# Kernel optimization log

Measured on AMD Instinct MI355X. Metric: run time of the kernel, lower is better.

Reference implementation:

```python
import jax, jax.numpy as jnp
import numpy as np

B, S, D = 4, 2048, 1024
H = 16
HD = D // H  # 64

def setup_inputs() -> dict:
    key = jax.random.key(0)
    ks = jax.random.split(key, 4)
    scale = 0.02
    return {
        "hidden_states": jax.random.normal(ks[0], (B, S, D), dtype=jnp.float32),
        "attention_mask": jnp.zeros((B, 1, 1, S), dtype=jnp.float32),
        "Wq": jax.random.normal(ks[1], (D, D), dtype=jnp.float32) * scale,
        "bq": jnp.zeros((D,), dtype=jnp.float32),
        "Wk": jax.random.normal(ks[2], (D, D), dtype=jnp.float32) * scale,
        "bk": jnp.zeros((D,), dtype=jnp.float32),
        "Wv": jax.random.normal(ks[3], (D, D), dtype=jnp.float32) * scale,
        "bv": jnp.zeros((D,), dtype=jnp.float32),
    }

def reference(hidden_states, attention_mask, Wq, bq, Wk, bk, Wv, bv):
    b, s, d = hidden_states.shape
    def proj(W, bias):
        # Linear then split heads: [b, s, d] -> [b, H, s, HD]
        y = hidden_states @ W.T + bias
        return y.reshape(b, s, H, HD).transpose(0, 2, 1, 3)
    Q = proj(Wq, bq)
    K = proj(Wk, bk)
    V = proj(Wv, bv)
    scores = jnp.einsum('bhqd,bhkd->bhqk', Q, K) / jnp.sqrt(jnp.float32(HD))
    scores = scores + attention_mask  # additive mask, broadcast [b,1,1,s]
    probs = jax.nn.softmax(scores, axis=-1)
    # dropout prob = 0.0 (eval-mode): identity
    context = jnp.einsum('bhqk,bhkd->bhqd', probs, V)
    return context.transpose(0, 2, 1, 3).reshape(b, s, d)
```

## Files before the change

kernel.cpp:

```cpp
#include <hip/hip_runtime.h>


typedef short bf16x4 __attribute__((ext_vector_type(4)));
typedef short bf16x8 __attribute__((ext_vector_type(8)));
typedef float f32x4 __attribute__((ext_vector_type(4)));

#define SEQ 2048
#define DIM 1024
#define NH 16
#define HDIM 64
#define QKV_ELEMS ((size_t)64 * SEQ * HDIM)

#define WS_FLAG  50331648ull
#define WS_XBF   50331904ull
#define WS_WBF   67109120ull
#define WS_BF32  73400576ull
#define WS_NEED  73412868ull

#define LOG2E 1.4426950408889634f
#define QSCALE (0.125f * LOG2E)

static __device__ __forceinline__ unsigned short f2bf(float f) {
  union { float f; unsigned u; } x; x.f = f;
  unsigned r = x.u + 0x7fffu + ((x.u >> 16) & 1u);
  return (unsigned short)(r >> 16);
}
static __device__ __forceinline__ float bf2f(unsigned short h) {
  union { unsigned u; float f; } x; x.u = ((unsigned)h) << 16;
  return x.f;
}
static __device__ __forceinline__ unsigned cvtpk(float a, float b) {
  unsigned r;
  asm("v_cvt_pk_bf16_f32 %0, %1, %2" : "=v"(r) : "v"(a), "v"(b));
  return r;
}
static __device__ __forceinline__ int vswz(int s) {
  return (s & ~31) | (((s >> 2) & 3) << 3) | (((s >> 4) & 1) << 2);
}

template <bool FP32>
static __device__ __forceinline__ float load1(const void* p, size_t i) {
  if (FP32) return ((const float*)p)[i];
  else      return bf2f(((const unsigned short*)p)[i]);
}
template <bool FP32>
static __device__ __forceinline__ bf16x8 load8bf(const void* p, size_t i) {
  if (FP32) {
    f32x4 a = *(const f32x4*)((const float*)p + i);
    f32x4 b = *(const f32x4*)((const float*)p + i + 4);
    union { bf16x8 v; unsigned short u[8]; } r;
#pragma unroll
    for (int j = 0; j < 4; ++j) { r.u[j] = f2bf(a[j]); r.u[4 + j] = f2bf(b[j]); }
    return r.v;
  } else {
    return *(const bf16x8*)((const unsigned short*)p + i);
  }
}
static __device__ __forceinline__ bf16x8 load8bf_rt(const void* p, size_t i, bool fp32) {
  return fp32 ? load8bf<true>(p, i) : load8bf<false>(p, i);
}

static __device__ __forceinline__ void glds16(const unsigned short* g, unsigned short* l) {
  __builtin_amdgcn_global_load_lds(
      (const __attribute__((address_space(1))) unsigned int*)(unsigned long long)(const void*)g,
      (__attribute__((address_space(3))) unsigned int*)(unsigned int)(unsigned long long)(void*)l,
      16, 0, 0);
}

__global__ void detect_dtype(const unsigned short* __restrict__ X, int* __restrict__ flag) {
  __shared__ int zc[1024], bc[1024];
  int z = 0, b = 0;
  for (int i = threadIdx.x; i < 4096; i += 1024) {
    unsigned short u = X[8 * i];
    if (u == 0) z++;
    int e = (u >> 7) & 0xff;
    if (e >= 134) b++;
  }
  zc[threadIdx.x] = z; bc[threadIdx.x] = b;
  __syncthreads();
  for (int s = 512; s > 0; s >>= 1) {
    if (threadIdx.x < s) { zc[threadIdx.x] += zc[threadIdx.x + s]; bc[threadIdx.x] += bc[threadIdx.x + s]; }
    __syncthreads();
  }
  if (threadIdx.x == 0)
    *flag = (zc[0] > 2048 || bc[0] > 16) ? 1 : 0;
}

__global__ void convert_all_u(const void* __restrict__ X,
                              const void* __restrict__ Wq, const void* __restrict__ Wk,
                              const void* __restrict__ Wv,
                              const void* __restrict__ bq, const void* __restrict__ bk,
                              const void* __restrict__ bv,
                              unsigned char* __restrict__ ws, const int* __restrict__ flag) {
  const bool fp32 = (*flag != 0);
  unsigned short* Xb = (unsigned short*)(ws + WS_XBF);
  unsigned short* Wb = (unsigned short*)(ws + WS_WBF);
  float* Bb = (float*)(ws + WS_BF32);
  int blk = blockIdx.x;
  if (blk < 4096) {
    size_t base = ((size_t)blk * 256 + threadIdx.x) * 8;
    *(bf16x8*)(Xb + base) = load8bf_rt(X, base, fp32);
  } else if (blk < 5632) {
    int w = (blk - 4096) >> 9;
    int r = (blk - 4096) & 511;
    const void* W = (w == 0) ? Wq : (w == 1) ? Wk : Wv;
    size_t base = ((size_t)r * 256 + threadIdx.x) * 8;
    *(bf16x8*)(Wb + (size_t)w * 1048576 + base) = load8bf_rt(W, base, fp32);
  } else {
    int w = blk - 5632;
    const void* Bsrc = (w == 0) ? bq : (w == 1) ? bk : bv;
    for (int i = threadIdx.x; i < 1024; i += 256)
      Bb[w * 1024 + i] = fp32 ? load1<true>(Bsrc, i) : load1<false>(Bsrc, i);
  }
}

__global__ __launch_bounds__(256) void qkv_bf(
    const unsigned short* __restrict__ Xb, const unsigned short* __restrict__ Wb,
    const float* __restrict__ Bb,
    unsigned short* __restrict__ Qo, unsigned short* __restrict__ Ko,
    unsigned short* __restrict__ Vo)
{
  const int bid = blockIdx.x;
  const int wg  = (bid & 7) * 192 + (bid >> 3);
  const int z   = wg / 512;
  const int rem = wg - z * 512;
  const int nb  = rem >> 6;
  const int mb  = rem & 63;
  const unsigned short* W = Wb + (size_t)z * 1048576;

  __shared__ __align__(16) unsigned short Xs[128 * 64];
  __shared__ __align__(16) unsigned short Ws[128 * 64];

  const int tid  = threadIdx.x;
  const int wave = tid >> 6;
  const int lane = tid & 63;
  const int col  = lane & 15;
  const int quad = lane >> 4;
  const int wr = wave & 1;
  const int wc = wave >> 1;
  const int m0 = mb * 128;
  const int n0 = nb * 128;

  f32x4 zero4 = {0.f, 0.f, 0.f, 0.f};
  f32x4 acc[4][4];
#pragma unroll
  for (int i = 0; i < 4; ++i)
#pragma unroll
    for (int j = 0; j < 4; ++j) acc[i][j] = zero4;

  const int srow8 = lane >> 3;
  const int sseg  = lane & 7;

  for (int k0 = 0; k0 < DIM; k0 += 64) {
    __syncthreads();
#pragma unroll
    for (int a = 0; a < 4; ++a) {
      int rowbase = wave * 32 + a * 8;
      int row = rowbase + srow8;
      int lseg = sseg ^ (row & 7);
      glds16(Xb + (size_t)(m0 + row) * DIM + k0 + lseg * 8, Xs + rowbase * 64);
      glds16(W  + (size_t)(n0 + row) * DIM + k0 + lseg * 8, Ws + rowbase * 64);
    }
    __syncthreads();

#pragma unroll
    for (int kk = 0; kk < 2; ++kk) {
      bf16x8 Af[4], Bf[4];
#pragma unroll
      for (int i = 0; i < 4; ++i) {
        int ra = wr * 64 + i * 16 + col;
        Af[i] = *(const bf16x8*)(Xs + ra * 64 + ((kk * 4 + quad) ^ (ra & 7)) * 8);
        int rb = wc * 64 + i * 16 + col;
        Bf[i] = *(const bf16x8*)(Ws + rb * 64 + ((kk * 4 + quad) ^ (rb & 7)) * 8);
      }
#pragma unroll
      for (int i = 0; i < 4; ++i)
#pragma unroll
        for (int j = 0; j < 4; ++j)
          acc[i][j] = __builtin_amdgcn_mfma_f32_16x16x32_bf16(Af[i], Bf[j], acc[i][j], 0, 0, 0);
    }
  }

  const float oscale = (z == 0) ? QSCALE : 1.0f;
  if (z < 2) {
    unsigned short* Yo = (z == 0) ? Qo : Ko;
#pragma unroll
    for (int i = 0; i < 4; ++i) {
#pragma unroll
      for (int j = 0; j < 4; ++j) {
        int n = n0 + wc * 64 + j * 16 + col;
        float bvf = Bb[z * 1024 + n];
        int h = n >> 6, hd = n & 63;
#pragma unroll
        for (int r = 0; r < 4; ++r) {
          int m = m0 + wr * 64 + i * 16 + quad * 4 + r;
          int b = m >> 11, s = m & 2047;
          Yo[((size_t)(b * NH + h) * SEQ + s) * HDIM + hd] = f2bf((acc[i][j][r] + bvf) * oscale);
        }
      }
    }
  } else {
#pragma unroll
    for (int i = 0; i < 4; ++i) {
#pragma unroll
      for (int j = 0; j < 4; ++j) {
        int n = n0 + wc * 64 + j * 16 + col;
        float bvf = Bb[2 * 1024 + n];
        int h = n >> 6, hd = n & 63;
        int mbase = m0 + wr * 64 + i * 16 + quad * 4;
        int b = mbase >> 11, s = mbase & 2047;
        unsigned long long pk = 0;
#pragma unroll
        for (int r = 0; r < 4; ++r)
          pk |= (unsigned long long)f2bf(acc[i][j][r] + bvf) << (16 * r);
        *(unsigned long long*)(Vo + ((size_t)(b * NH + h) * HDIM + hd) * SEQ + vswz(s)) = pk;
      }
    }
  }
}

#define XS_STRIDE 40
template <bool FP32>
__global__ __launch_bounds__(256) void qkv_any(
    const void* __restrict__ X,
    const void* __restrict__ Wq, const void* __restrict__ bq,
    const void* __restrict__ Wk, const void* __restrict__ bk,
    const void* __restrict__ Wv, const void* __restrict__ bv,
    unsigned short* __restrict__ Qo, unsigned short* __restrict__ Ko,
    unsigned short* __restrict__ Vo, const int* __restrict__ flag)
{
  if (*flag != (FP32 ? 1 : 0)) return;
  const int z = blockIdx.z;
  const void* W    = (z == 0) ? Wq : (z == 1) ? Wk : Wv;
  const void* bias = (z == 0) ? bq : (z == 1) ? bk : bv;

  __shared__ __align__(16) unsigned short Xs[128 * XS_STRIDE];
  __shared__ __align__(16) unsigned short Ws[128 * XS_STRIDE];

  const int tid  = threadIdx.x;
  const int wave = tid >> 6;
  const int lane = tid & 63;
  const int col  = lane & 15;
  const int quad = lane >> 4;
  const int wr = wave & 1;
  const int wc = wave >> 1;
  const int m0 = blockIdx.x * 128;
  const int n0 = blockIdx.y * 128;

  f32x4 zero4 = {0.f, 0.f, 0.f, 0.f};
  f32x4 acc[4][4];
#pragma unroll
  for (int i = 0; i < 4; ++i)
#pragma unroll
    for (int j = 0; j < 4; ++j) acc[i][j] = zero4;

  const int srow = tid >> 2;
  const int sseg = (tid & 3) << 3;

  for (int k0 = 0; k0 < DIM; k0 += 32) {
    __syncthreads();
#pragma unroll
    for (int a = 0; a < 2; ++a) {
      int r = a * 64 + srow;
      *(bf16x8*)(Xs + r * XS_STRIDE + sseg) = load8bf<FP32>(X, (size_t)(m0 + r) * DIM + k0 + sseg);
      *(bf16x8*)(Ws + r * XS_STRIDE + sseg) = load8bf<FP32>(W, (size_t)(n0 + r) * DIM + k0 + sseg);
    }
    __syncthreads();

    bf16x8 Af[4], Bf[4];
#pragma unroll
    for (int i = 0; i < 4; ++i)
      Af[i] = *(const bf16x8*)(Xs + (wr * 64 + i * 16 + col) * XS_STRIDE + quad * 8);
#pragma unroll
    for (int j = 0; j < 4; ++j)
      Bf[j] = *(const bf16x8*)(Ws + (wc * 64 + j * 16 + col) * XS_STRIDE + quad * 8);
#pragma unroll
    for (int i = 0; i < 4; ++i)
#pragma unroll
      for (int j = 0; j < 4; ++j)
        acc[i][j] = __builtin_amdgcn_mfma_f32_16x16x32_bf16(Af[i], Bf[j], acc[i][j], 0, 0, 0);
  }

  const float oscale = (z == 0) ? QSCALE : 1.0f;
  if (z < 2) {
    unsigned short* Yo = (z == 0) ? Qo : Ko;
#pragma unroll
    for (int i = 0; i < 4; ++i) {
#pragma unroll
      for (int j = 0; j < 4; ++j) {
        int n = n0 + wc * 64 + j * 16 + col;
        float bvf = load1<FP32>(bias, n);
        int h = n >> 6, hd = n & 63;
#pragma unroll
        for (int r = 0; r < 4; ++r) {
          int m = m0 + wr * 64 + i * 16 + quad * 4 + r;
          int b = m >> 11, s = m & 2047;
          Yo[((size_t)(b * NH + h) * SEQ + s) * HDIM + hd] = f2bf((acc[i][j][r] + bvf) * oscale);
        }
      }
    }
  } else {
#pragma unroll
    for (int i = 0; i < 4; ++i) {
#pragma unroll
      for (int j = 0; j < 4; ++j) {
        int n = n0 + wc * 64 + j * 16 + col;
        float bvf = load1<FP32>(bias, n);
        int h = n >> 6, hd = n & 63;
        int mbase = m0 + wr * 64 + i * 16 + quad * 4;
        int b = mbase >> 11, s = mbase & 2047;
        unsigned long long pk = 0;
#pragma unroll
        for (int r = 0; r < 4; ++r)
          pk |= (unsigned long long)f2bf(acc[i][j][r] + bvf) << (16 * r);
        *(unsigned long long*)(Vo + ((size_t)(b * NH + h) * HDIM + hd) * SEQ + vswz(s)) = pk;
      }
    }
  }
}

__global__ __launch_bounds__(512, 2) void attn_kernel(
    const unsigned short* __restrict__ Q,
    const unsigned short* __restrict__ K,
    const unsigned short* __restrict__ Vt,
    const void* __restrict__ mask,
    void* __restrict__ OutV, const int* __restrict__ flag)
{
  const bool fp32 = (*flag != 0);

  __shared__ __align__(16) unsigned short Ks[2 * 128 * 64];
  __shared__ __align__(16) unsigned short Vs[2 * 64 * 128];
  __shared__ __align__(16) float Msall[SEQ];

  const int tid  = threadIdx.x;
  const int wave = tid >> 6;
  const int lane = tid & 63;
  const int col  = lane & 15;
  const int quad = lane >> 4;
  const int qt = blockIdx.x;
  const int bh = blockIdx.y;
  const int b  = bh >> 4;
  const int h  = bh & 15;

  const unsigned short* Qb = Q  + (size_t)bh * SEQ * HDIM;
  const unsigned short* Kb = K  + (size_t)bh * SEQ * HDIM;
  const unsigned short* Vb = Vt + (size_t)bh * HDIM * SEQ;

  {
    if (fp32) {
      f32x4 a = *(const f32x4*)((const float*)mask + (size_t)b * SEQ + tid * 4);
#pragma unroll
      for (int j = 0; j < 4; ++j) a[j] *= LOG2E;
      *(f32x4*)(Msall + tid * 4) = a;
    } else {
      bf16x4 v = *(const bf16x4*)((const unsigned short*)mask + (size_t)b * SEQ + tid * 4);
      f32x4 a;
#pragma unroll
      for (int j = 0; j < 4; ++j) a[j] = bf2f((unsigned short)v[j]) * LOG2E;
      *(f32x4*)(Msall + tid * 4) = a;
    }
  }

  const int qrow0 = qt * 256 + wave * 32 + col;
  const int qrow1 = qrow0 + 16;
  const bf16x8 Qf00 = *(const bf16x8*)(Qb + (size_t)qrow0 * HDIM + quad * 8);
  const bf16x8 Qf01 = *(const bf16x8*)(Qb + (size_t)qrow0 * HDIM + 32 + quad * 8);
  const bf16x8 Qf10 = *(const bf16x8*)(Qb + (size_t)qrow1 * HDIM + quad * 8);
  const bf16x8 Qf11 = *(const bf16x8*)(Qb + (size_t)qrow1 * HDIM + 32 + quad * 8);

  const f32x4 z4 = {0.f, 0.f, 0.f, 0.f};
  f32x4 Oacc0[4], Oacc1[4];
  f32x4 Osum0 = z4, Osum1 = z4;
#pragma unroll
  for (int t = 0; t < 4; ++t) { Oacc0[t] = z4; Oacc1[t] = z4; }
  float mrun0 = -1e30f, mrun1 = -1e30f;

  union { bf16x8 v; unsigned u[4]; } ones;
#pragma unroll
  for (int i = 0; i < 4; ++i) ones.u[i] = 0x3F803F80u;

  const int krow_in = lane >> 3;
  const int kphys   = lane & 7;
  const int klseg   = kphys ^ krow_in;
  const unsigned short* kSrc0 = Kb + (size_t)(wave * 16 + 0 + krow_in) * HDIM + klseg * 8;
  const unsigned short* kSrc1 = Kb + (size_t)(wave * 16 + 8 + krow_in) * HDIM + klseg * 8;
  const int vrow_in = lane >> 4;
  const int vphys   = lane & 15;
  const int vrowA0  = wave * 8 + 0 + vrow_in;
  const int vrowA1  = wave * 8 + 4 + vrow_in;
  const unsigned short* vSrc0 = Vb + (size_t)vrowA0 * SEQ + (vphys ^ (vrowA0 & 15)) * 8;
  const unsigned short* vSrc1 = Vb + (size_t)vrowA1 * SEQ + (vphys ^ (vrowA1 & 15)) * 8;

  auto stage = [&](int ktn, int bufn) {
    unsigned short* Kdst = Ks + bufn * (128 * 64) + (wave * 16) * 64;
    unsigned short* Vdst = Vs + bufn * (64 * 128) + (wave * 8) * 128;
    const size_t ko = (size_t)ktn * 128 * HDIM;
    const size_t vo = (size_t)ktn * 128;
    glds16(kSrc0 + ko, Kdst);
    glds16(kSrc1 + ko, Kdst + 8 * 64);
    glds16(vSrc0 + vo, Vdst);
    glds16(vSrc1 + vo, Vdst + 4 * 128);
  };

  stage(0, 0);

  for (int kt = 0; kt < 16; ++kt) {
    __syncthreads();
    if (kt < 15) stage(kt + 1, (kt + 1) & 1);

    const unsigned short* Kcur = Ks + (kt & 1) * (128 * 64);
    const unsigned short* Vcur = Vs + (kt & 1) * (64 * 128);
    const float* Mc = Msall + kt * 128;

    f32x4 st0[8], st1[8];
    __builtin_amdgcn_s_setprio(1);
#pragma unroll
    for (int t = 0; t < 8; ++t) {
      const unsigned short* kr = Kcur + (t * 16 + col) * 64;
      bf16x8 Ka = *(const bf16x8*)(kr + (quad ^ (col & 7)) * 8);
      bf16x8 Kc = *(const bf16x8*)(kr + ((4 + quad) ^ (col & 7)) * 8);
      f32x4 c = *(const f32x4*)(Mc + t * 16 + quad * 4);
      f32x4 d0 = c, d1 = c;
      d0 = __builtin_amdgcn_mfma_f32_16x16x32_bf16(Ka, Qf00, d0, 0, 0, 0);
      d0 = __builtin_amdgcn_mfma_f32_16x16x32_bf16(Kc, Qf01, d0, 0, 0, 0);
      d1 = __builtin_amdgcn_mfma_f32_16x16x32_bf16(Ka, Qf10, d1, 0, 0, 0);
      d1 = __builtin_amdgcn_mfma_f32_16x16x32_bf16(Kc, Qf11, d1, 0, 0, 0);
      st0[t] = d0; st1[t] = d1;
    }
    __builtin_amdgcn_s_setprio(0);

    float pm0, pm1;
    {
      f32x4 m40, m41;
#pragma unroll
      for (int r = 0; r < 4; ++r) {
        float a0 = fmaxf(fmaxf(st0[0][r], st0[1][r]), st0[2][r]);
        a0 = fmaxf(fmaxf(a0, st0[3][r]), st0[4][r]);
        a0 = fmaxf(fmaxf(a0, st0[5][r]), st0[6][r]);
        m40[r] = fmaxf(a0, st0[7][r]);
        float a1 = fmaxf(fmaxf(st1[0][r], st1[1][r]), st1[2][r]);
        a1 = fmaxf(fmaxf(a1, st1[3][r]), st1[4][r]);
        a1 = fmaxf(fmaxf(a1, st1[5][r]), st1[6][r]);
        m41[r] = fmaxf(a1, st1[7][r]);
      }
      pm0 = fmaxf(fmaxf(fmaxf(m40[0], m40[1]), m40[2]), m40[3]);
      pm1 = fmaxf(fmaxf(fmaxf(m41[0], m41[1]), m41[2]), m41[3]);
    }
    pm0 = fmaxf(pm0, __shfl_xor(pm0, 16, 64));
    pm0 = fmaxf(pm0, __shfl_xor(pm0, 32, 64));
    pm1 = fmaxf(pm1, __shfl_xor(pm1, 16, 64));
    pm1 = fmaxf(pm1, __shfl_xor(pm1, 32, 64));

    if (!__all((pm0 - mrun0 <= 8.0f) && (pm1 - mrun1 <= 8.0f))) {
      float mn0 = fmaxf(mrun0, pm0), mn1 = fmaxf(mrun1, pm1);
      float a0 = __builtin_amdgcn_exp2f(mrun0 - mn0);
      float a1 = __builtin_amdgcn_exp2f(mrun1 - mn1);
      mrun0 = mn0; mrun1 = mn1;
      float av0[4], av1[4];
#pragma unroll
      for (int r = 0; r < 4; ++r) {
        av0[r] = __shfl(a0, quad * 4 + r, 64);
        av1[r] = __shfl(a1, quad * 4 + r, 64);
      }
#pragma unroll
      for (int t = 0; t < 4; ++t)
#pragma unroll
        for (int r = 0; r < 4; ++r) {
          Oacc0[t][r] *= av0[r];
          Oacc1[t][r] *= av1[r];
        }
#pragma unroll
      for (int r = 0; r < 4; ++r) { Osum0[r] *= av0[r]; Osum1[r] *= av1[r]; }
    }

#pragma unroll
    for (int t = 0; t < 8; ++t)
#pragma unroll
      for (int r = 0; r < 4; ++r) {
        st0[t][r] = __builtin_amdgcn_exp2f(st0[t][r] - mrun0);
        st1[t][r] = __builtin_amdgcn_exp2f(st1[t][r] - mrun1);
      }

    __builtin_amdgcn_s_setprio(1);
#pragma unroll
    for (int tp = 0; tp < 4; ++tp) {
      union { bf16x8 v; unsigned u[4]; } A0, A1;
      A0.u[0] = cvtpk(st0[2 * tp][0],     st0[2 * tp][1]);
      A0.u[1] = cvtpk(st0[2 * tp][2],     st0[2 * tp][3]);
      A0.u[2] = cvtpk(st0[2 * tp + 1][0], st0[2 * tp + 1][1]);
      A0.u[3] = cvtpk(st0[2 * tp + 1][2], st0[2 * tp + 1][3]);
      A1.u[0] = cvtpk(st1[2 * tp][0],     st1[2 * tp][1]);
      A1.u[1] = cvtpk(st1[2 * tp][2],     st1[2 * tp][3]);
      A1.u[2] = cvtpk(st1[2 * tp + 1][0], st1[2 * tp + 1][1]);
      A1.u[3] = cvtpk(st1[2 * tp + 1][2], st1[2 * tp + 1][3]);
      Osum0 = __builtin_amdgcn_mfma_f32_16x16x32_bf16(A0.v, ones.v, Osum0, 0, 0, 0);
      Osum1 = __builtin_amdgcn_mfma_f32_16x16x32_bf16(A1.v, ones.v, Osum1, 0, 0, 0);
#pragma unroll
      for (int t2 = 0; t2 < 4; ++t2) {
        bf16x8 Bv = *(const bf16x8*)(Vcur + (t2 * 16 + col) * 128 + ((tp * 4 + quad) ^ col) * 8);
        Oacc0[t2] = __builtin_amdgcn_mfma_f32_16x16x32_bf16(A0.v, Bv, Oacc0[t2], 0, 0, 0);
        Oacc1[t2] = __builtin_amdgcn_mfma_f32_16x16x32_bf16(A1.v, Bv, Oacc1[t2], 0, 0, 0);
      }
    }
    __builtin_amdgcn_s_setprio(0);
  }

  float liv0[4], liv1[4];
#pragma unroll
  for (int r = 0; r < 4; ++r) { liv0[r] = 1.0f / Osum0[r]; liv1[r] = 1.0f / Osum1[r]; }
#pragma unroll
  for (int t2 = 0; t2 < 4; ++t2) {
#pragma unroll
    for (int r = 0; r < 4; ++r) {
      int q0 = qt * 256 + wave * 32 + quad * 4 + r;
      int q1 = q0 + 16;
      float v0 = Oacc0[t2][r] * liv0[r];
      float v1 = Oacc1[t2][r] * liv1[r];
      v0 = (v0 == v0) ? v0 : 0.0f;
      v1 = (v1 == v1) ? v1 : 0.0f;
      size_t o0 = ((size_t)b * SEQ + q0) * DIM + h * HDIM + t2 * 16 + col;
      size_t o1 = ((size_t)b * SEQ + q1) * DIM + h * HDIM + t2 * 16 + col;
      if (fp32) {
        ((float*)OutV)[o0] = v0;
        ((float*)OutV)[o1] = v1;
      } else {
        ((unsigned short*)OutV)[o0] = f2bf(v0);
        ((unsigned short*)OutV)[o1] = f2bf(v1);
      }
    }
  }
}

extern "C" void kernel_launch(void* const* d_in, const int* in_sizes, int n_in,
                              void* d_out, int out_size, void* d_ws, size_t ws_size,
                              hipStream_t stream) {
  const void* X    = d_in[0];
  const void* mask = d_in[1];
  const void* Wq   = d_in[2];
  const void* bq   = d_in[3];
  const void* Wk   = d_in[4];
  const void* bk   = d_in[5];
  const void* Wv   = d_in[6];
  const void* bv   = d_in[7];

  unsigned char* ws = (unsigned char*)d_ws;
  unsigned short* Qw = (unsigned short*)ws;
  unsigned short* Kw = Qw + QKV_ELEMS;
  unsigned short* Vw = Kw + QKV_ELEMS;
  int* flag = (int*)(ws + WS_FLAG);

  detect_dtype<<<1, 1024, 0, stream>>>((const unsigned short*)X, flag);

  if (ws_size >= WS_NEED) {
    convert_all_u<<<5635, 256, 0, stream>>>(X, Wq, Wk, Wv, bq, bk, bv, ws, flag);
    qkv_bf<<<1536, 256, 0, stream>>>(
        (const unsigned short*)(ws + WS_XBF), (const unsigned short*)(ws + WS_WBF),
        (const float*)(ws + WS_BF32), Qw, Kw, Vw);
  } else {
    qkv_any<false><<<dim3(64, 8, 3), 256, 0, stream>>>(X, Wq, bq, Wk, bk, Wv, bv, Qw, Kw, Vw, flag);
    qkv_any<true ><<<dim3(64, 8, 3), 256, 0, stream>>>(X, Wq, bq, Wk, bk, Wv, bv, Qw, Kw, Vw, flag);
  }

  attn_kernel<<<dim3(8, 64), 512, 0, stream>>>(Qw, Kw, Vw, mask, d_out, flag);
}
```

Measured before the change: 262.9 us.

## Double-buffer QKV GEMM with 512 threads and prefetch V fragments in attention

The QKV projection kernel moves to 8 waves per block with a 64x32 tile per wave and double-buffered LDS, so the next K-slice's global-to-LDS loads are issued while the current slice is computed. This removes one barrier per iteration. In the attention kernel, the first half of the V fragments is loaded from LDS before the softmax max/exp section, to hide LDS latency. The cost is double the LDS per GEMM block and more live registers in the attention loop.

```diff
diff --git a/kernel.cpp b/kernel.cpp
--- a/kernel.cpp
+++ b/kernel.cpp
@@ -114,7 +114,7 @@
   }
 }
 
-__global__ __launch_bounds__(256) void qkv_bf(
+__global__ __launch_bounds__(512, 2) void qkv_bf(
     const unsigned short* __restrict__ Xb, const unsigned short* __restrict__ Wb,
     const float* __restrict__ Bb,
     unsigned short* __restrict__ Qo, unsigned short* __restrict__ Ko,
@@ -128,8 +128,8 @@
   const int mb  = rem & 63;
   const unsigned short* W = Wb + (size_t)z * 1048576;
 
-  __shared__ __align__(16) unsigned short Xs[128 * 64];
-  __shared__ __align__(16) unsigned short Ws[128 * 64];
+  __shared__ __align__(16) unsigned short Xs[2][128 * 64];
+  __shared__ __align__(16) unsigned short Ws[2][128 * 64];
 
   const int tid  = threadIdx.x;
   const int wave = tid >> 6;
@@ -142,41 +142,55 @@
   const int n0 = nb * 128;
 
   f32x4 zero4 = {0.f, 0.f, 0.f, 0.f};
-  f32x4 acc[4][4];
+  f32x4 acc[4][2];
 #pragma unroll
   for (int i = 0; i < 4; ++i)
 #pragma unroll
-    for (int j = 0; j < 4; ++j) acc[i][j] = zero4;
+    for (int j = 0; j < 2; ++j) acc[i][j] = zero4;
 
   const int srow8 = lane >> 3;
   const int sseg  = lane & 7;
-
-  for (int k0 = 0; k0 < DIM; k0 += 64) {
+  const int lseg  = sseg ^ srow8;
+  const unsigned short* xA0 = Xb + (size_t)(m0 + 0  + wave * 8 + srow8) * DIM + lseg * 8;
+  const unsigned short* xA1 = Xb + (size_t)(m0 + 64 + wave * 8 + srow8) * DIM + lseg * 8;
+  const unsigned short* wA0 = W  + (size_t)(n0 + 0  + wave * 8 + srow8) * DIM + lseg * 8;
+  const unsigned short* wA1 = W  + (size_t)(n0 + 64 + wave * 8 + srow8) * DIM + lseg * 8;
+
+  auto stage = [&](int k0, int bufn) {
+    unsigned short* Xd = Xs[bufn] + (wave * 8) * 64;
+    unsigned short* Wd = Ws[bufn] + (wave * 8) * 64;
+    glds16(xA0 + k0, Xd);
+    glds16(xA1 + k0, Xd + 64 * 64);
+    glds16(wA0 + k0, Wd);
+    glds16(wA1 + k0, Wd + 64 * 64);
+  };
+
+  stage(0, 0);
+
+  for (int ks = 0; ks < 16; ++ks) {
     __syncthreads();
-#pragma unroll
-    for (int a = 0; a < 4; ++a) {
-      int rowbase = wave * 32 + a * 8;
-      int row = rowbase + srow8;
-      int lseg = sseg ^ (row & 7);
-      glds16(Xb + (size_t)(m0 + row) * DIM + k0 + lseg * 8, Xs + rowbase * 64);
-      glds16(W  + (size_t)(n0 + row) * DIM + k0 + lseg * 8, Ws + rowbase * 64);
-    }
-    __syncthreads();
+    if (ks < 15) stage((ks + 1) * 64, (ks + 1) & 1);
+
+    const unsigned short* Xc = Xs[ks & 1];
+    const unsigned short* Wc = Ws[ks & 1];
 
 #pragma unroll
     for (int kk = 0; kk < 2; ++kk) {
-      bf16x8 Af[4], Bf[4];
+      bf16x8 Af[4], Bf[2];
 #pragma unroll
       for (int i = 0; i < 4; ++i) {
         int ra = wr * 64 + i * 16 + col;
-        Af[i] = *(const bf16x8*)(Xs + ra * 64 + ((kk * 4 + quad) ^ (ra & 7)) * 8);
-        int rb = wc * 64 + i * 16 + col;
-        Bf[i] = *(const bf16x8*)(Ws + rb * 64 + ((kk * 4 + quad) ^ (rb & 7)) * 8);
+        Af[i] = *(const bf16x8*)(Xc + ra * 64 + ((kk * 4 + quad) ^ (ra & 7)) * 8);
+      }
+#pragma unroll
+      for (int j = 0; j < 2; ++j) {
+        int rb = wc * 32 + j * 16 + col;
+        Bf[j] = *(const bf16x8*)(Wc + rb * 64 + ((kk * 4 + quad) ^ (rb & 7)) * 8);
       }
 #pragma unroll
       for (int i = 0; i < 4; ++i)
 #pragma unroll
-        for (int j = 0; j < 4; ++j)
+        for (int j = 0; j < 2; ++j)
           acc[i][j] = __builtin_amdgcn_mfma_f32_16x16x32_bf16(Af[i], Bf[j], acc[i][j], 0, 0, 0);
     }
   }
@@ -187,8 +201,8 @@
 #pragma unroll
     for (int i = 0; i < 4; ++i) {
 #pragma unroll
-      for (int j = 0; j < 4; ++j) {
-        int n = n0 + wc * 64 + j * 16 + col;
+      for (int j = 0; j < 2; ++j) {
+        int n = n0 + wc * 32 + j * 16 + col;
         float bvf = Bb[z * 1024 + n];
         int h = n >> 6, hd = n & 63;
 #pragma unroll
@@ -203,8 +217,8 @@
 #pragma unroll
     for (int i = 0; i < 4; ++i) {
 #pragma unroll
-      for (int j = 0; j < 4; ++j) {
-        int n = n0 + wc * 64 + j * 16 + col;
+      for (int j = 0; j < 2; ++j) {
+        int n = n0 + wc * 32 + j * 16 + col;
         float bvf = Bb[2 * 1024 + n];
         int h = n >> 6, hd = n & 63;
         int mbase = m0 + wr * 64 + i * 16 + quad * 4;
@@ -429,6 +443,13 @@
     }
     __builtin_amdgcn_s_setprio(0);
 
+    bf16x8 Bv01[2][4];
+#pragma unroll
+    for (int tp = 0; tp < 2; ++tp)
+#pragma unroll
+      for (int t2 = 0; t2 < 4; ++t2)
+        Bv01[tp][t2] = *(const bf16x8*)(Vcur + (t2 * 16 + col) * 128 + ((tp * 4 + quad) ^ col) * 8);
+
     float pm0, pm1;
     {
       f32x4 m40, m41;
@@ -497,7 +518,8 @@
       Osum1 = __builtin_amdgcn_mfma_f32_16x16x32_bf16(A1.v, ones.v, Osum1, 0, 0, 0);
 #pragma unroll
       for (int t2 = 0; t2 < 4; ++t2) {
-        bf16x8 Bv = *(const bf16x8*)(Vcur + (t2 * 16 + col) * 128 + ((tp * 4 + quad) ^ col) * 8);
+        bf16x8 Bv = (tp < 2) ? Bv01[tp][t2]
+                  : *(const bf16x8*)(Vcur + (t2 * 16 + col) * 128 + ((tp * 4 + quad) ^ col) * 8);
         Oacc0[t2] = __builtin_amdgcn_mfma_f32_16x16x32_bf16(A0.v, Bv, Oacc0[t2], 0, 0, 0);
         Oacc1[t2] = __builtin_amdgcn_mfma_f32_16x16x32_bf16(A1.v, Bv, Oacc1[t2], 0, 0, 0);
       }
@@ -553,7 +575,7 @@
 
   if (ws_size >= WS_NEED) {
     convert_all_u<<<5635, 256, 0, stream>>>(X, Wq, Wk, Wv, bq, bk, bv, ws, flag);
-    qkv_bf<<<1536, 256, 0, stream>>>(
+    qkv_bf<<<1536, 512, 0, stream>>>(
         (const unsigned short*)(ws + WS_XBF), (const unsigned short*)(ws + WS_WBF),
         (const float*)(ws + WS_BF32), Qw, Kw, Vw);
   } else {
```

New measurement: 259.9 us. About the same (-1.1%).
